# Kernel tuning notes

Measured on AMD Instinct MI355X. Metric: run time of the kernel, lower is better.

Reference implementation:

```python
import jax, jax.numpy as jnp
import numpy as np

D_INNER = 1024
STATE = 16
DT_RANK = 64  # ceil(d_inner / 16)
LOG_EPS = -7.0
CLAMP = 20.0


def setup_inputs() -> dict:
    key = jax.random.key(0)
    ks = jax.random.split(key, 4)
    B, L = 2, 1024
    x = jax.random.normal(ks[0], (B, L, D_INNER), jnp.float32)
    # x_proj: Linear(d_inner -> dt_rank + 2*state_size, bias=False); stored as (in, out)
    W_xproj = jax.random.normal(ks[1], (D_INNER, DT_RANK + 2 * STATE), jnp.float32) * 0.02
    # dt_proj: Linear(dt_rank -> d_inner, bias=True)
    W_dt = jax.random.normal(ks[2], (DT_RANK, D_INNER), jnp.float32) * 0.02
    b_dt = jax.random.normal(ks[3], (D_INNER,), jnp.float32) * 0.02
    # A_log = log(arange(1..state_size)) repeated over d_inner rows
    A_log = jnp.log(jnp.tile(jnp.arange(1, STATE + 1, dtype=jnp.float32), (D_INNER, 1)))
    D = jnp.ones((D_INNER,), jnp.float32)
    return {"x": x, "W_xproj": W_xproj, "W_dt": W_dt, "b_dt": b_dt, "A_log": A_log, "D": D}


def reference(x, W_xproj, W_dt, b_dt, A_log, D):
    # x: (B, L, d_inner)
    proj = x @ W_xproj  # (B, L, dt_rank + 2*N)
    dt_inter = proj[..., :DT_RANK]
    B_ssm = proj[..., DT_RANK:DT_RANK + STATE]   # (B, L, N)
    C_ssm = proj[..., DT_RANK + STATE:]          # (B, L, N)

    delta = jax.nn.softplus(dt_inter @ W_dt + b_dt)  # (B, L, d_inner)

    # discretization (ZOH)
    A = -jnp.exp(A_log)  # (d_inner, N), negative
    log_delta_A = jnp.clip(delta[..., None] * A[None, None], LOG_EPS, CLAMP)
    delta_A = jnp.exp(log_delta_A)                              # (B, L, d, N)
    delta_B_u = (delta[..., None] * B_ssm[:, :, None, :]) * x[..., None]  # (B, L, d, N)

    # log-space cumsum scan
    log_dA = jnp.log(jnp.clip(delta_A, 1e-7, None))
    log_R = jnp.cumsum(log_dA, axis=1)
    R = jnp.exp(jnp.minimum(log_R, CLAMP))
    exp_neg_log_R = jnp.exp(jnp.minimum(-log_R, CLAMP))
    S = jnp.cumsum(delta_B_u * exp_neg_log_R, axis=1)
    h = R * S  # (B, L, d, N)

    y = jnp.einsum('bln,bldn->bld', C_ssm, h) + x * D
    return y
```

## Files before the change

### kernel.cpp

```cpp
#include <hip/hip_runtime.h>
#include <math.h>

#define D_INNER 1024
#define STATE   16
#define DT_RANK 64
#define NPROJ   96
#define LSEQ    1024
#define NBATCH  2

#define LOG2E   1.4426950408889634f
#define NEG7L2  (-7.0f * LOG2E)
#define P20L2   (20.0f * LOG2E)

template<int CTRL, int RMASK>
__device__ __forceinline__ float dppadd(float v) {
    int t = __builtin_amdgcn_update_dpp(0, __float_as_int(v), CTRL, RMASK, 0xf, false);
    return v + __int_as_float(t);
}
__device__ __forceinline__ float wave_iscan(float v) {
    v = dppadd<0x111, 0xf>(v);
    v = dppadd<0x112, 0xf>(v);
    v = dppadd<0x114, 0xf>(v);
    v = dppadd<0x118, 0xf>(v);
    v = dppadd<0x142, 0xa>(v);
    v = dppadd<0x143, 0xc>(v);
    return v;
}

__global__ __launch_bounds__(768) void proj_kernel(
        const float* __restrict__ x, const float* __restrict__ Wx,
        float* __restrict__ projdt, float* __restrict__ Bg, float* __restrict__ Cg) {
    const int tid = threadIdx.x;
    const int j  = tid % 96;
    const int kq = tid / 96;
    const int row0 = blockIdx.x * 8;

    __shared__ float xs[8 * 1024];
    __shared__ float red[8][8][96];

    {
        const float4* src = (const float4*)(x + (size_t)row0 * 1024);
        #pragma unroll
        for (int i = 0; i < 3; ++i) {
            int idx = tid + 768 * i;
            if (idx < 2048) {
                float4 v = src[idx];
                *(float4*)&xs[idx * 4] = v;
            }
        }
    }
    __syncthreads();

    const float* wp = Wx + (size_t)(kq * 128) * 96 + j;
    const float* xk = &xs[kq * 128];

    float a[8];
    #pragma unroll
    for (int r = 0; r < 8; ++r) a[r] = 0.f;

    #pragma unroll 8
    for (int k = 0; k < 128; ++k) {
        float w = wp[(size_t)k * 96];
        #pragma unroll
        for (int r = 0; r < 8; ++r)
            a[r] = fmaf(xk[r * 1024 + k], w, a[r]);
    }

    #pragma unroll
    for (int r = 0; r < 8; ++r) red[kq][r][j] = a[r];
    __syncthreads();

    {
        const int r  = tid / 96;
        const int jj = tid % 96;
        float s = 0.f;
        #pragma unroll
        for (int p = 0; p < 8; ++p) s += red[p][r][jj];
        const int row = row0 + r;
        const int b = row >> 10, l = row & 1023;
        if (jj < 64)      projdt[(size_t)row * 64 + jj] = s;
        else if (jj < 80) Bg[((size_t)b * 16 + (jj - 64)) * 1024 + l] = s;
        else              Cg[((size_t)b * 16 + (jj - 80)) * 1024 + l] = s;
    }
}

__global__ __launch_bounds__(256) void delta_kernel(
        const float* __restrict__ projdt, const float* __restrict__ Wdt,
        const float* __restrict__ bdt, const float* __restrict__ x,
        float* __restrict__ delta_t, float* __restrict__ u_t) {
    const int bid = blockIdx.x;
    const int lt = bid >> 4;
    const int dt = bid & 15;
    const int row0 = lt * 64;
    const int d0 = dt * 64;
    const int tid = threadIdx.x;

    __shared__ float pl[64][69];
    __shared__ float wlbuf[64 * 68];
    __shared__ float dtile[64][65];
    float (*wl)[68] = (float(*)[68])wlbuf;

    {
        const float4* src = (const float4*)(projdt + (size_t)row0 * 64);
        #pragma unroll
        for (int i = 0; i < 4; ++i) {
            int f4i = tid + 256 * i;
            float4 v = src[f4i];
            int l = f4i >> 4, k4 = (f4i & 15) << 2;
            pl[l][k4+0] = v.x; pl[l][k4+1] = v.y; pl[l][k4+2] = v.z; pl[l][k4+3] = v.w;
        }
    }
    {
        #pragma unroll
        for (int i = 0; i < 4; ++i) {
            int f4i = tid + 256 * i;
            int k = f4i >> 4, m4 = (f4i & 15) << 2;
            float4 v = *(const float4*)(Wdt + (size_t)k * 1024 + d0 + m4);
            *(float4*)&wl[k][m4] = v;
        }
    }
    __syncthreads();

    const int lsub = tid & 63;
    const int dq = tid >> 6;
    float acc[16];
    #pragma unroll
    for (int i = 0; i < 16; ++i) acc[i] = 0.f;

    #pragma unroll 4
    for (int k = 0; k < 64; ++k) {
        float p = pl[lsub][k];
        const float4* wr = (const float4*)&wl[k][dq * 16];
        float4 w0 = wr[0], w1 = wr[1], w2 = wr[2], w3 = wr[3];
        acc[0]  = fmaf(p, w0.x, acc[0]);  acc[1]  = fmaf(p, w0.y, acc[1]);
        acc[2]  = fmaf(p, w0.z, acc[2]);  acc[3]  = fmaf(p, w0.w, acc[3]);
        acc[4]  = fmaf(p, w1.x, acc[4]);  acc[5]  = fmaf(p, w1.y, acc[5]);
        acc[6]  = fmaf(p, w1.z, acc[6]);  acc[7]  = fmaf(p, w1.w, acc[7]);
        acc[8]  = fmaf(p, w2.x, acc[8]);  acc[9]  = fmaf(p, w2.y, acc[9]);
        acc[10] = fmaf(p, w2.z, acc[10]); acc[11] = fmaf(p, w2.w, acc[11]);
        acc[12] = fmaf(p, w3.x, acc[12]); acc[13] = fmaf(p, w3.y, acc[13]);
        acc[14] = fmaf(p, w3.z, acc[14]); acc[15] = fmaf(p, w3.w, acc[15]);
    }

    #pragma unroll
    for (int i = 0; i < 16; ++i) {
        float v = acc[i] + bdt[d0 + dq * 16 + i];
        float sp = fmaxf(v, 0.f) + log1pf(__expf(-fabsf(v)));
        dtile[dq * 16 + i][lsub] = sp;
    }
    __syncthreads();

    float (*xs)[65] = (float(*)[65])wlbuf;
    {
        #pragma unroll
        for (int i = 0; i < 4; ++i) {
            int f4i = tid + 256 * i;
            int l = f4i >> 4, m4 = (f4i & 15) << 2;
            float4 v = *(const float4*)(x + (size_t)(row0 + l) * 1024 + d0 + m4);
            xs[l][m4+0] = v.x; xs[l][m4+1] = v.y; xs[l][m4+2] = v.z; xs[l][m4+3] = v.w;
        }
    }
    __syncthreads();

    {
        int dp_ = tid >> 2, seg = tid & 3;
        int b = row0 >> 10, l0 = row0 & 1023;
        size_t off = ((size_t)b * 1024 + d0 + dp_) * 1024 + l0 + seg * 16;
        float* ddst = delta_t + off;
        float* udst = u_t + off;
        #pragma unroll
        for (int m = 0; m < 4; ++m) {
            int lb = seg * 16 + m * 4;
            float4 v;
            v.x = dtile[dp_][lb + 0];
            v.y = dtile[dp_][lb + 1];
            v.z = dtile[dp_][lb + 2];
            v.w = dtile[dp_][lb + 3];
            float4 u;
            u.x = v.x * xs[lb + 0][dp_];
            u.y = v.y * xs[lb + 1][dp_];
            u.z = v.z * xs[lb + 2][dp_];
            u.w = v.w * xs[lb + 3][dp_];
            ((float4*)ddst)[m] = v;
            ((float4*)udst)[m] = u;
        }
    }
}

__global__ __launch_bounds__(512, 4) void scan_kernel(
        const float* __restrict__ delta_t, const float* __restrict__ u_t,
        const float* __restrict__ Bg, const float* __restrict__ Cg,
        const float* __restrict__ A_log, const float* __restrict__ Dvec,
        float* __restrict__ yout) {
    const int bid0 = blockIdx.x;
    const int bid  = (bid0 & 7) * 64 + (bid0 >> 3);
    const int wv   = threadIdx.x >> 6;
    const int ch   = wv >> 1;
    const int half = wv & 1;
    const int lane = threadIdx.x & 63;
    const int chain = bid * 4 + ch;
    const int b = chain >> 10;
    const int d = chain & 1023;
    const int l0 = lane * 16;

    __shared__ float ycomb[4][64][17];
    __shared__ float T[4][1088];

    const size_t choff = ((size_t)b * 1024 + d) * 1024 + l0;

    float dl[16], ul[16];
    #pragma unroll
    for (int k = 0; k < 4; ++k) {
        float4 v = *(const float4*)(delta_t + choff + k * 4);
        dl[4*k+0] = v.x; dl[4*k+1] = v.y; dl[4*k+2] = v.z; dl[4*k+3] = v.w;
    }
    #pragma unroll
    for (int k = 0; k < 4; ++k) {
        float4 v = *(const float4*)(u_t + choff + k * 4);
        ul[4*k+0] = v.x; ul[4*k+1] = v.y; ul[4*k+2] = v.z; ul[4*k+3] = v.w;
    }

    const float* Bp = Bg + (size_t)b * 16 * 1024 + l0;
    const float* Cp = Cg + (size_t)b * 16 * 1024 + l0;

    float y[16];
    if (half == 0) {
        const float Dd = Dvec[d];
        #pragma unroll
        for (int l = 0; l < 16; ++l)
            y[l] = ul[l] * __builtin_amdgcn_rcpf(dl[l]) * Dd;
    } else {
        #pragma unroll
        for (int l = 0; l < 16; ++l) y[l] = 0.f;
    }

    #pragma unroll 1
    for (int jn = 0; jn < 8; ++jn) {
        const int n = half * 8 + jn;
        const float a = -__expf(A_log[d * 16 + n]) * LOG2E;

        float local = 0.f;
        #pragma unroll
        for (int l = 0; l < 16; ++l)
            local += fmaxf(dl[l] * a, NEG7L2);
        float incl = wave_iscan(local);
        float c = incl - local;

        float Bv[16], Cv[16];
        #pragma unroll
        for (int k = 0; k < 4; ++k) {
            float4 bv = *(const float4*)(Bp + (size_t)n * 1024 + k * 4);
            Bv[4*k+0] = bv.x; Bv[4*k+1] = bv.y; Bv[4*k+2] = bv.z; Bv[4*k+3] = bv.w;
            float4 cv = *(const float4*)(Cp + (size_t)n * 1024 + k * 4);
            Cv[4*k+0] = cv.x; Cv[4*k+1] = cv.y; Cv[4*k+2] = cv.z; Cv[4*k+3] = cv.w;
        }

        float g[16];
        float srun = 0.f;
        #pragma unroll
        for (int l = 0; l < 16; ++l) {
            c += fmaxf(dl[l] * a, NEG7L2);
            g[l] = Cv[l] * exp2f(c);
            srun = fmaf(ul[l] * Bv[l], exp2f(fminf(-c, P20L2)), srun);
            y[l] = fmaf(g[l], srun, y[l]);
        }

        float incl2 = wave_iscan(srun);
        float lex = incl2 - srun;
        #pragma unroll
        for (int l = 0; l < 16; ++l)
            y[l] = fmaf(g[l], lex, y[l]);
    }

    if (half == 1) {
        #pragma unroll
        for (int l = 0; l < 16; ++l)
            ycomb[ch][lane][l] = y[l];
    }
    __syncthreads();
    if (half == 0) {
        #pragma unroll
        for (int k = 0; k < 16; ++k) {
            int l = l0 + k;
            T[ch][l + (l >> 4)] = y[k] + ycomb[ch][lane][k];
        }
    }
    __syncthreads();

    {
        const int d0 = (bid * 4) & 1023;
        float* yb = yout + (size_t)b * 1024 * 1024 + d0;
        #pragma unroll
        for (int m = 0; m < 2; ++m) {
            int l = threadIdx.x * 2 + m;
            int sw = l + (l >> 4);
            float4 o = make_float4(T[0][sw], T[1][sw], T[2][sw], T[3][sw]);
            *(float4*)(yb + (size_t)l * 1024) = o;
        }
    }
}

extern "C" void kernel_launch(void* const* d_in, const int* in_sizes, int n_in,
                              void* d_out, int out_size, void* d_ws, size_t ws_size,
                              hipStream_t stream) {
    const float* x    = (const float*)d_in[0];
    const float* Wx   = (const float*)d_in[1];
    const float* Wdt  = (const float*)d_in[2];
    const float* bdt  = (const float*)d_in[3];
    const float* Alog = (const float*)d_in[4];
    const float* Dvec = (const float*)d_in[5];
    float* y = (float*)d_out;

    float* projdt  = (float*)d_ws;
    float* Bgp     = projdt + (size_t)2048 * 64;
    float* Cgp     = Bgp + (size_t)2 * 16 * 1024;
    float* delta_t = Cgp + (size_t)2 * 16 * 1024;
    float* u_t     = delta_t + (size_t)2 * 1024 * 1024;

    proj_kernel<<<256, 768, 0, stream>>>(x, Wx, projdt, Bgp, Cgp);
    delta_kernel<<<512, 256, 0, stream>>>(projdt, Wdt, bdt, x, delta_t, u_t);
    scan_kernel<<<512, 512, 0, stream>>>(delta_t, u_t, Bgp, Cgp, Alog, Dvec, y);
}
```

Measured before the change: 70.35 us.

## Fuse x_proj and dt_proj/softplus into one kernel, dropping projdt round trip

Merges the projection kernel and the delta kernel. Each 8-row block keeps its dt-rank slice in shared memory and computes delta = softplus(p·W_dt + b) and u = delta·x directly, reusing the x tile already loaded. This removes one kernel launch, the global write and read of projdt, and a second read of x. In exchange each block now rereads all of W_dt (256 KB) from global or L2 for only 8 rows, and writes only 8 contiguous floats per d row in delta_t/u_t, which is less coalesced.

Result: faster. 66.12 us (-6.0%).

```diff
diff --git a/kernel.cpp b/kernel.cpp
--- a/kernel.cpp
+++ b/kernel.cpp
@@ -27,9 +27,11 @@
     return v;
 }
 
-__global__ __launch_bounds__(768) void proj_kernel(
+__global__ __launch_bounds__(768) void projdelta_kernel(
         const float* __restrict__ x, const float* __restrict__ Wx,
-        float* __restrict__ projdt, float* __restrict__ Bg, float* __restrict__ Cg) {
+        const float* __restrict__ Wdt, const float* __restrict__ bdt,
+        float* __restrict__ Bg, float* __restrict__ Cg,
+        float* __restrict__ delta_t, float* __restrict__ u_t) {
     const int tid = threadIdx.x;
     const int j  = tid % 96;
     const int kq = tid / 96;
@@ -37,6 +39,7 @@
 
     __shared__ float xs[8 * 1024];
     __shared__ float red[8][8][96];
+    __shared__ float pdl[8][64];
 
     {
         const float4* src = (const float4*)(x + (size_t)row0 * 1024);
@@ -51,23 +54,25 @@
     }
     __syncthreads();
 
-    const float* wp = Wx + (size_t)(kq * 128) * 96 + j;
-    const float* xk = &xs[kq * 128];
-
-    float a[8];
-    #pragma unroll
-    for (int r = 0; r < 8; ++r) a[r] = 0.f;
-
-    #pragma unroll 8
-    for (int k = 0; k < 128; ++k) {
-        float w = wp[(size_t)k * 96];
-        #pragma unroll
-        for (int r = 0; r < 8; ++r)
-            a[r] = fmaf(xk[r * 1024 + k], w, a[r]);
-    }
-
-    #pragma unroll
-    for (int r = 0; r < 8; ++r) red[kq][r][j] = a[r];
+    {
+        const float* wp = Wx + (size_t)(kq * 128) * 96 + j;
+        const float* xk = &xs[kq * 128];
+
+        float a[8];
+        #pragma unroll
+        for (int r = 0; r < 8; ++r) a[r] = 0.f;
+
+        #pragma unroll 8
+        for (int k = 0; k < 128; ++k) {
+            float w = wp[(size_t)k * 96];
+            #pragma unroll
+            for (int r = 0; r < 8; ++r)
+                a[r] = fmaf(xk[r * 1024 + k], w, a[r]);
+        }
+
+        #pragma unroll
+        for (int r = 0; r < 8; ++r) red[kq][r][j] = a[r];
+    }
     __syncthreads();
 
     {
@@ -78,111 +83,61 @@
         for (int p = 0; p < 8; ++p) s += red[p][r][jj];
         const int row = row0 + r;
         const int b = row >> 10, l = row & 1023;
-        if (jj < 64)      projdt[(size_t)row * 64 + jj] = s;
+        if (jj < 64)      pdl[r][jj] = s;
         else if (jj < 80) Bg[((size_t)b * 16 + (jj - 64)) * 1024 + l] = s;
         else              Cg[((size_t)b * 16 + (jj - 80)) * 1024 + l] = s;
     }
-}
-
-__global__ __launch_bounds__(256) void delta_kernel(
-        const float* __restrict__ projdt, const float* __restrict__ Wdt,
-        const float* __restrict__ bdt, const float* __restrict__ x,
-        float* __restrict__ delta_t, float* __restrict__ u_t) {
-    const int bid = blockIdx.x;
-    const int lt = bid >> 4;
-    const int dt = bid & 15;
-    const int row0 = lt * 64;
-    const int d0 = dt * 64;
-    const int tid = threadIdx.x;
-
-    __shared__ float pl[64][69];
-    __shared__ float wlbuf[64 * 68];
-    __shared__ float dtile[64][65];
-    float (*wl)[68] = (float(*)[68])wlbuf;
-
-    {
-        const float4* src = (const float4*)(projdt + (size_t)row0 * 64);
-        #pragma unroll
-        for (int i = 0; i < 4; ++i) {
-            int f4i = tid + 256 * i;
-            float4 v = src[f4i];
-            int l = f4i >> 4, k4 = (f4i & 15) << 2;
-            pl[l][k4+0] = v.x; pl[l][k4+1] = v.y; pl[l][k4+2] = v.z; pl[l][k4+3] = v.w;
-        }
-    }
-    {
-        #pragma unroll
-        for (int i = 0; i < 4; ++i) {
-            int f4i = tid + 256 * i;
-            int k = f4i >> 4, m4 = (f4i & 15) << 2;
-            float4 v = *(const float4*)(Wdt + (size_t)k * 1024 + d0 + m4);
-            *(float4*)&wl[k][m4] = v;
-        }
-    }
-    __syncthreads();
-
-    const int lsub = tid & 63;
-    const int dq = tid >> 6;
-    float acc[16];
-    #pragma unroll
-    for (int i = 0; i < 16; ++i) acc[i] = 0.f;
-
-    #pragma unroll 4
-    for (int k = 0; k < 64; ++k) {
-        float p = pl[lsub][k];
-        const float4* wr = (const float4*)&wl[k][dq * 16];
-        float4 w0 = wr[0], w1 = wr[1], w2 = wr[2], w3 = wr[3];
-        acc[0]  = fmaf(p, w0.x, acc[0]);  acc[1]  = fmaf(p, w0.y, acc[1]);
-        acc[2]  = fmaf(p, w0.z, acc[2]);  acc[3]  = fmaf(p, w0.w, acc[3]);
-        acc[4]  = fmaf(p, w1.x, acc[4]);  acc[5]  = fmaf(p, w1.y, acc[5]);
-        acc[6]  = fmaf(p, w1.z, acc[6]);  acc[7]  = fmaf(p, w1.w, acc[7]);
-        acc[8]  = fmaf(p, w2.x, acc[8]);  acc[9]  = fmaf(p, w2.y, acc[9]);
-        acc[10] = fmaf(p, w2.z, acc[10]); acc[11] = fmaf(p, w2.w, acc[11]);
-        acc[12] = fmaf(p, w3.x, acc[12]); acc[13] = fmaf(p, w3.y, acc[13]);
-        acc[14] = fmaf(p, w3.z, acc[14]); acc[15] = fmaf(p, w3.w, acc[15]);
-    }
-
-    #pragma unroll
-    for (int i = 0; i < 16; ++i) {
-        float v = acc[i] + bdt[d0 + dq * 16 + i];
-        float sp = fmaxf(v, 0.f) + log1pf(__expf(-fabsf(v)));
-        dtile[dq * 16 + i][lsub] = sp;
-    }
-    __syncthreads();
-
-    float (*xs)[65] = (float(*)[65])wlbuf;
-    {
-        #pragma unroll
-        for (int i = 0; i < 4; ++i) {
-            int f4i = tid + 256 * i;
-            int l = f4i >> 4, m4 = (f4i & 15) << 2;
-            float4 v = *(const float4*)(x + (size_t)(row0 + l) * 1024 + d0 + m4);
-            xs[l][m4+0] = v.x; xs[l][m4+1] = v.y; xs[l][m4+2] = v.z; xs[l][m4+3] = v.w;
-        }
-    }
-    __syncthreads();
-
-    {
-        int dp_ = tid >> 2, seg = tid & 3;
-        int b = row0 >> 10, l0 = row0 & 1023;
-        size_t off = ((size_t)b * 1024 + d0 + dp_) * 1024 + l0 + seg * 16;
-        float* ddst = delta_t + off;
-        float* udst = u_t + off;
-        #pragma unroll
-        for (int m = 0; m < 4; ++m) {
-            int lb = seg * 16 + m * 4;
-            float4 v;
-            v.x = dtile[dp_][lb + 0];
-            v.y = dtile[dp_][lb + 1];
-            v.z = dtile[dp_][lb + 2];
-            v.w = dtile[dp_][lb + 3];
-            float4 u;
-            u.x = v.x * xs[lb + 0][dp_];
-            u.y = v.y * xs[lb + 1][dp_];
-            u.z = v.z * xs[lb + 2][dp_];
-            u.w = v.w * xs[lb + 3][dp_];
-            ((float4*)ddst)[m] = v;
-            ((float4*)udst)[m] = u;
+    __syncthreads();
+
+    const int b  = row0 >> 10;
+    const int l0 = row0 & 1023;
+    #pragma unroll 1
+    for (int it = 0; it < 2; ++it) {
+        const int d = tid + it * 768;
+        if (d < 1024) {
+            const float bb = bdt[d];
+            float acc[8];
+            #pragma unroll
+            for (int r = 0; r < 8; ++r) acc[r] = bb;
+
+            #pragma unroll 1
+            for (int c = 0; c < 4; ++c) {
+                float w[16];
+                #pragma unroll
+                for (int kk = 0; kk < 16; ++kk)
+                    w[kk] = Wdt[(size_t)(c * 16 + kk) * 1024 + d];
+                #pragma unroll
+                for (int r = 0; r < 8; ++r) {
+                    const float4 p0 = *(const float4*)&pdl[r][c * 16 + 0];
+                    const float4 p1 = *(const float4*)&pdl[r][c * 16 + 4];
+                    const float4 p2 = *(const float4*)&pdl[r][c * 16 + 8];
+                    const float4 p3 = *(const float4*)&pdl[r][c * 16 + 12];
+                    float t = acc[r];
+                    t = fmaf(p0.x, w[0],  t); t = fmaf(p0.y, w[1],  t);
+                    t = fmaf(p0.z, w[2],  t); t = fmaf(p0.w, w[3],  t);
+                    t = fmaf(p1.x, w[4],  t); t = fmaf(p1.y, w[5],  t);
+                    t = fmaf(p1.z, w[6],  t); t = fmaf(p1.w, w[7],  t);
+                    t = fmaf(p2.x, w[8],  t); t = fmaf(p2.y, w[9],  t);
+                    t = fmaf(p2.z, w[10], t); t = fmaf(p2.w, w[11], t);
+                    t = fmaf(p3.x, w[12], t); t = fmaf(p3.y, w[13], t);
+                    t = fmaf(p3.z, w[14], t); t = fmaf(p3.w, w[15], t);
+                    acc[r] = t;
+                }
+            }
+
+            float od[8], ou[8];
+            #pragma unroll
+            for (int r = 0; r < 8; ++r) {
+                float v = acc[r];
+                float sp = fmaxf(v, 0.f) + log1pf(__expf(-fabsf(v)));
+                od[r] = sp;
+                ou[r] = sp * xs[r * 1024 + d];
+            }
+            const size_t off = ((size_t)b * 1024 + d) * 1024 + l0;
+            *(float4*)(delta_t + off)     = make_float4(od[0], od[1], od[2], od[3]);
+            *(float4*)(delta_t + off + 4) = make_float4(od[4], od[5], od[6], od[7]);
+            *(float4*)(u_t + off)     = make_float4(ou[0], ou[1], ou[2], ou[3]);
+            *(float4*)(u_t + off + 4) = make_float4(ou[4], ou[5], ou[6], ou[7]);
         }
     }
 }
@@ -311,13 +266,11 @@
     const float* Dvec = (const float*)d_in[5];
     float* y = (float*)d_out;
 
-    float* projdt  = (float*)d_ws;
-    float* Bgp     = projdt + (size_t)2048 * 64;
+    float* Bgp     = (float*)d_ws;
     float* Cgp     = Bgp + (size_t)2 * 16 * 1024;
     float* delta_t = Cgp + (size_t)2 * 16 * 1024;
     float* u_t     = delta_t + (size_t)2 * 1024 * 1024;
 
-    proj_kernel<<<256, 768, 0, stream>>>(x, Wx, projdt, Bgp, Cgp);
-    delta_kernel<<<512, 256, 0, stream>>>(projdt, Wdt, bdt, x, delta_t, u_t);
+    projdelta_kernel<<<256, 768, 0, stream>>>(x, Wx, Wdt, bdt, Bgp, Cgp, delta_t, u_t);
     scan_kernel<<<512, 512, 0, stream>>>(delta_t, u_t, Bgp, Cgp, Alog, Dvec, y);
 }
```
